# Kernel tuning notes

Measured on AMD Instinct MI355X. Metric: run time of the kernel, lower is better.

## Reference

```python
import jax, jax.numpy as jnp
import numpy as np

MARGIN = 0.3
NORM_EPS = 1e-12  # torch F.normalize default eps


def setup_inputs() -> dict:
    key = jax.random.key(0)
    k1, k2 = jax.random.split(key)
    embeddings = jax.random.normal(k1, (8192, 128), dtype=jnp.float32)
    labels = jax.random.randint(k2, (8192,), 0, 128, dtype=jnp.int64)
    return {"embeddings": embeddings, "labels": labels}


def _triplet_loss(embeddings, labels):
    # L2-normalize rows (torch F.normalize: x / max(||x||, eps))
    norm = jnp.linalg.norm(embeddings, axis=1, keepdims=True)
    e = embeddings / jnp.maximum(norm, NORM_EPS)

    # pairwise squared Euclidean via gram matrix
    dot = e @ e.T                     # [B, B]
    sq = jnp.diagonal(dot)            # [B]
    d2 = jnp.clip(sq[None, :] - 2.0 * dot + sq[:, None], 0.0)
    zmask = (d2 == 0.0).astype(d2.dtype)
    dist = jnp.sqrt(d2 + zmask * 1e-16) * (1.0 - zmask)  # [B, B]

    # hard mining, fully vectorized over rows
    same = labels[:, None] == labels[None, :]
    eye = jnp.eye(labels.shape[0], dtype=bool)
    pos_mask = same & ~eye
    neg_mask = ~same

    dist_ap = jnp.max(jnp.where(pos_mask, dist, -jnp.inf), axis=1)  # hardest positive
    dist_an = jnp.min(jnp.where(neg_mask, dist, jnp.inf), axis=1)   # hardest negative

    valid = pos_mask.any(axis=1) & neg_mask.any(axis=1)
    # MarginRankingLoss(margin)(dist_an, dist_ap, y=1) = mean relu(dist_ap - dist_an + margin)
    per_row = jnp.maximum(dist_ap - dist_an + MARGIN, 0.0)
    n_valid = jnp.maximum(jnp.sum(valid), 1).astype(dist.dtype)
    loss = jnp.sum(jnp.where(valid, per_row, 0.0)) / n_valid
    return jnp.where(valid.any(), loss, jnp.zeros((), dist.dtype))


def reference(embeddings, labels):
    return _triplet_loss(embeddings, labels)
```

## Files before the change

### kernel.cpp

```cpp
#include <hip/hip_runtime.h>
#include <cmath>

#define BN 8192
#define DIM 128
#define MARGIN_F 0.3f
#define NRB 64
#define NTILE (NRB * (NRB + 1) / 2)
#define NPART 64
#define IMAX 0x7FFFFFFF
#define IMIN 0x80000000

typedef __attribute__((ext_vector_type(4))) int i32x4;

__device__ __forceinline__ int imin3(int a, int b, int c) { return min(a, min(b, c)); }
__device__ __forceinline__ int imax3(int a, int b, int c) { return max(a, max(b, c)); }

__global__ __launch_bounds__(256) void norm_cvt_k(
    const float* __restrict__ emb, const int* __restrict__ lab,
    float* __restrict__ sqv, unsigned short* __restrict__ EnQ16,
    unsigned* __restrict__ LP)
{
  int gt = blockIdx.x * blockDim.x + threadIdx.x;
  if (gt < 2048) {
    int base = (gt >> 4) * 64 + (gt & 15);
    LP[gt] = (unsigned)(lab[base] & 255) | ((unsigned)(lab[base + 16] & 255) << 8) |
             ((unsigned)(lab[base + 32] & 255) << 16) | ((unsigned)(lab[base + 48] & 255) << 24);
  }

  int w = gt >> 6;
  int lane = threadIdx.x & 63;
  if (w >= BN) return;
  float2 v = *reinterpret_cast<const float2*>(&emb[w * DIM + lane * 2]);
  float s = v.x * v.x + v.y * v.y;
  #pragma unroll
  for (int off = 32; off > 0; off >>= 1) s += __shfl_xor(s, off);
  float iv = 1.0f / fmaxf(sqrtf(s), 1e-12f);
  if (lane == 0) sqv[w] = s * iv * iv;
  int q0 = (int)rintf(127.0f * v.x * iv);
  int q1 = (int)rintf(127.0f * v.y * iv);
  unsigned short us = (unsigned short)((q0 & 255) | ((q1 & 255) << 8));
  int g = lane >> 3;
  EnQ16[(g * BN + w) * 8 + (lane & 7)] = us;
}

__global__ __launch_bounds__(256, 2) void tri_gram_mine_k(
    const char* __restrict__ EnQ, const int* __restrict__ lab,
    const unsigned* __restrict__ LP,
    int* __restrict__ ap_part, int* __restrict__ an_part)
{
  __shared__ int sRP[2][128], sRN[2][128];
  __shared__ int sCP[2][128], sCN[2][128];

  const int tid = threadIdx.x;
  const int w = tid >> 6, l = tid & 63;
  const int wr = w >> 1, wc = w & 1;
  const int lrow = l & 15, lkg = l >> 4;

  const int idx = blockIdx.x;
  int R = (int)((129.0f - sqrtf(16641.0f - 8.0f * (float)idx)) * 0.5f);
  while (((R + 1) * (129 - (R + 1))) / 2 <= idx) ++R;
  while ((R * (129 - R)) / 2 > idx) --R;
  const int C = R + (idx - (R * (129 - R)) / 2);

  const int rowBase = R * 128 + wr * 64;
  const int colBase = C * 128 + wc * 64;
  const bool diagW  = (rowBase == colBase);
  const bool doCol  = (R != C);

  i32x4 a[4][2];
  #pragma unroll
  for (int mi = 0; mi < 4; ++mi)
    #pragma unroll
    for (int kk = 0; kk < 2; ++kk)
      a[mi][kk] = *reinterpret_cast<const i32x4*>(
          EnQ + (((size_t)((kk << 2) + lkg) * BN + rowBase + mi * 16 + lrow) << 4));

  int rlv[4][4];
  #pragma unroll
  for (int mi = 0; mi < 4; ++mi) {
    int rb = rowBase + mi * 16 + lkg * 4;
    #pragma unroll
    for (int r = 0; r < 4; ++r) rlv[mi][r] = lab[rb + r] & 255;
  }

  const unsigned LPv = LP[(colBase >> 6) * 16 + lrow];
  const int l0 = (int)(LPv & 255u),         l1 = (int)((LPv >> 8) & 255u);
  const int l2 = (int)((LPv >> 16) & 255u), l3 = (int)(LPv >> 24);

  int ap[4][4], an[4][4];
  #pragma unroll
  for (int mi = 0; mi < 4; ++mi)
    #pragma unroll
    for (int r = 0; r < 4; ++r) { ap[mi][r] = IMAX; an[mi][r] = IMIN; }
  int cmin[4], cmax[4];
  #pragma unroll
  for (int n = 0; n < 4; ++n) { cmin[n] = IMAX; cmax[n] = IMIN; }

  const i32x4 zf = {0, 0, 0, 0};

  const char* bp0 = EnQ + (((size_t)lkg * BN + colBase + lrow) << 4);
  const char* bp1 = bp0 + ((size_t)BN << 6);

  i32x4 b0[2][2], b1[2][2];
  #pragma unroll
  for (int n = 0; n < 2; ++n) {
    b0[0][n] = *reinterpret_cast<const i32x4*>(bp0 + n * 256);
    b0[1][n] = *reinterpret_cast<const i32x4*>(bp1 + n * 256);
    b1[0][n] = *reinterpret_cast<const i32x4*>(bp0 + (2 + n) * 256);
    b1[1][n] = *reinterpret_cast<const i32x4*>(bp1 + (2 + n) * 256);
  }

  i32x4 accA[4][2], accB[4][2];
  #pragma unroll
  for (int mi = 0; mi < 4; ++mi)
    #pragma unroll
    for (int n = 0; n < 2; ++n)
      accA[mi][n] = __builtin_amdgcn_mfma_i32_16x16x64_i8(a[mi][0], b0[0][n], zf, 0, 0, 0);
  #pragma unroll
  for (int mi = 0; mi < 4; ++mi)
    #pragma unroll
    for (int n = 0; n < 2; ++n)
      accA[mi][n] = __builtin_amdgcn_mfma_i32_16x16x64_i8(a[mi][1], b0[1][n], accA[mi][n], 0, 0, 0);
  #pragma unroll
  for (int mi = 0; mi < 4; ++mi)
    #pragma unroll
    for (int n = 0; n < 2; ++n)
      accB[mi][n] = __builtin_amdgcn_mfma_i32_16x16x64_i8(a[mi][0], b1[0][n], zf, 0, 0, 0);
  #pragma unroll
  for (int mi = 0; mi < 4; ++mi)
    #pragma unroll
    for (int n = 0; n < 2; ++n)
      accB[mi][n] = __builtin_amdgcn_mfma_i32_16x16x64_i8(a[mi][1], b1[1][n], accB[mi][n], 0, 0, 0);

  auto mineRow = [&](const i32x4 (&A)[4][2], int la, int lb) {
    #pragma unroll
    for (int mi = 0; mi < 4; ++mi)
      #pragma unroll
      for (int r = 0; r < 4; ++r) {
        int d0 = A[mi][0][r], d1 = A[mi][1][r];
        bool s0 = (rlv[mi][r] == la), s1 = (rlv[mi][r] == lb);
        int p0 = s0 ? d0 : IMAX, p1 = s1 ? d1 : IMAX;
        int q0 = s0 ? IMIN : d0, q1 = s1 ? IMIN : d1;
        ap[mi][r] = imin3(ap[mi][r], p0, p1);
        an[mi][r] = imax3(an[mi][r], q0, q1);
      }
  };
  auto mineRowCol = [&](const i32x4 (&A)[4][2], int la, int lb,
                        int& cmA, int& cxA, int& cmB, int& cxB) {
    #pragma unroll
    for (int mi = 0; mi < 4; ++mi)
      #pragma unroll
      for (int r = 0; r < 4; ++r) {
        int d0 = A[mi][0][r], d1 = A[mi][1][r];
        bool s0 = (rlv[mi][r] == la), s1 = (rlv[mi][r] == lb);
        int p0 = s0 ? d0 : IMAX, p1 = s1 ? d1 : IMAX;
        int q0 = s0 ? IMIN : d0, q1 = s1 ? IMIN : d1;
        ap[mi][r] = imin3(ap[mi][r], p0, p1);
        an[mi][r] = imax3(an[mi][r], q0, q1);
        cmA = min(cmA, p0); cxA = max(cxA, q0);
        cmB = min(cmB, p1); cxB = max(cxB, q1);
      }
  };
  auto mineDiag = [&](const i32x4 (&A)[4][2], int la, int lb, int c0, int c1) {
    #pragma unroll
    for (int mi = 0; mi < 4; ++mi)
      #pragma unroll
      for (int r = 0; r < 4; ++r) {
        int rloc = mi * 16 + lkg * 4 + r;
        int d0 = A[mi][0][r], d1 = A[mi][1][r];
        bool s0 = (rlv[mi][r] == la), s1 = (rlv[mi][r] == lb);
        bool e0 = (rloc == c0), e1 = (rloc == c1);
        int p0 = (s0 && !e0) ? d0 : IMAX, p1 = (s1 && !e1) ? d1 : IMAX;
        int q0 = s0 ? IMIN : d0, q1 = s1 ? IMIN : d1;
        ap[mi][r] = imin3(ap[mi][r], p0, p1);
        an[mi][r] = imax3(an[mi][r], q0, q1);
      }
  };

  if (diagW) {
    mineDiag(accA, l0, l1, lrow, 16 + lrow);
    mineDiag(accB, l2, l3, 32 + lrow, 48 + lrow);
  } else if (doCol) {
    mineRowCol(accA, l0, l1, cmin[0], cmax[0], cmin[1], cmax[1]);
    mineRowCol(accB, l2, l3, cmin[2], cmax[2], cmin[3], cmax[3]);
  } else {
    mineRow(accA, l0, l1);
    mineRow(accB, l2, l3);
  }

  #pragma unroll
  for (int mi = 0; mi < 4; ++mi)
    #pragma unroll
    for (int r = 0; r < 4; ++r) {
      int p = ap[mi][r], n = an[mi][r];
      #pragma unroll
      for (int off = 1; off < 16; off <<= 1) {
        p = min(p, __shfl_xor(p, off));
        n = max(n, __shfl_xor(n, off));
      }
      if (lrow == 0) {
        int rl = wr * 64 + mi * 16 + lkg * 4 + r;
        sRP[wc][rl] = p; sRN[wc][rl] = n;
      }
    }

  if (doCol) {
    #pragma unroll
    for (int n = 0; n < 4; ++n) {
      int cm = cmin[n], cx = cmax[n];
      cm = min(cm, __shfl_xor(cm, 16)); cm = min(cm, __shfl_xor(cm, 32));
      cx = max(cx, __shfl_xor(cx, 16)); cx = max(cx, __shfl_xor(cx, 32));
      if (lkg == 0) {
        int cl = wc * 64 + n * 16 + lrow;
        sCP[wr][cl] = cm; sCN[wr][cl] = cx;
      }
    }
  }

  __syncthreads();

  const int t = tid & 127;
  if (tid < 128) {
    int p = min(sRP[0][t], sRP[1][t]);
    int n = max(sRN[0][t], sRN[1][t]);
    ap_part[(size_t)C * BN + R * 128 + t] = p;
    an_part[(size_t)C * BN + R * 128 + t] = n;
  } else if (doCol) {
    int p = min(sCP[0][t], sCP[1][t]);
    int n = max(sCN[0][t], sCN[1][t]);
    ap_part[(size_t)R * BN + C * 128 + t] = p;
    an_part[(size_t)R * BN + C * 128 + t] = n;
  }
}

__global__ __launch_bounds__(256) void finalize_a_k(
    const int* __restrict__ ap_part, const int* __restrict__ an_part,
    const float* __restrict__ sqv,
    float* __restrict__ blk_sum, float* __restrict__ blk_cnt)
{
  __shared__ int sP[128], sN[128];
  __shared__ float ssum[4], scnt[4];
  const int tid = threadIdx.x;
  const int t = tid & 127, h = tid >> 7;
  const int r = blockIdx.x * 128 + t;

  int apt = IMAX, ant = IMIN;
  const int s0 = h * 32;
  #pragma unroll 8
  for (int s = 0; s < 32; ++s) {
    apt = min(apt, ap_part[(size_t)(s0 + s) * BN + r]);
    ant = max(ant, an_part[(size_t)(s0 + s) * BN + r]);
  }
  if (h) { sP[t] = apt; sN[t] = ant; }
  __syncthreads();

  float sum = 0.f, cnt = 0.f;
  if (!h) {
    apt = min(apt, sP[t]); ant = max(ant, sN[t]);
    if (apt != IMAX && ant != IMIN) {
      const float sc = 2.0f / (127.0f * 127.0f);
      float rs1 = sqv[r] + 1.0f;
      float dap = sqrtf(fmaxf(fmaf(-sc, (float)apt, rs1), 0.f));
      float dan = sqrtf(fmaxf(fmaf(-sc, (float)ant, rs1), 0.f));
      sum = fmaxf(dap - dan + MARGIN_F, 0.f);
      cnt = 1.f;
    }
  }
  #pragma unroll
  for (int off = 32; off > 0; off >>= 1) {
    sum += __shfl_xor(sum, off);
    cnt += __shfl_xor(cnt, off);
  }
  int wv = tid >> 6;
  if ((tid & 63) == 0) { ssum[wv] = sum; scnt[wv] = cnt; }
  __syncthreads();
  if (tid == 0) {
    blk_sum[blockIdx.x] = ssum[0] + ssum[1] + ssum[2] + ssum[3];
    blk_cnt[blockIdx.x] = scnt[0] + scnt[1] + scnt[2] + scnt[3];
  }
}

__global__ __launch_bounds__(64) void finalize_b_k(
    const float* __restrict__ blk_sum, const float* __restrict__ blk_cnt,
    float* __restrict__ out)
{
  int l = threadIdx.x;
  float s = blk_sum[l], c = blk_cnt[l];
  #pragma unroll
  for (int off = 32; off > 0; off >>= 1) {
    s += __shfl_xor(s, off);
    c += __shfl_xor(c, off);
  }
  if (l == 0) out[0] = (c > 0.f) ? (s / c) : 0.f;
}

extern "C" void kernel_launch(void* const* d_in, const int* in_sizes, int n_in,
                              void* d_out, int out_size, void* d_ws, size_t ws_size,
                              hipStream_t stream)
{
  const float* emb = (const float*)d_in[0];
  const int*   lab = (const int*)d_in[1];
  float* out = (float*)d_out;
  float* ws  = (float*)d_ws;

  float*    sqv     = ws;
  int*      ap_part = (int*)(sqv + BN);
  int*      an_part = ap_part + NPART * BN;
  float*    blk_sum = (float*)(an_part + NPART * BN);
  float*    blk_cnt = blk_sum + 64;
  unsigned* LP      = (unsigned*)(blk_cnt + 64);
  char*     EnQ     = (char*)(LP + 2048);

  norm_cvt_k<<<dim3(BN / 4), 256, 0, stream>>>(emb, lab, sqv, (unsigned short*)EnQ, LP);
  tri_gram_mine_k<<<dim3(NTILE), 256, 0, stream>>>(EnQ, lab, LP, ap_part, an_part);
  finalize_a_k<<<dim3(NRB), 256, 0, stream>>>(ap_part, an_part, sqv, blk_sum, blk_cnt);
  finalize_b_k<<<dim3(1), 64, 0, stream>>>(blk_sum, blk_cnt, out);
}
```

Baseline: 38.90 us.

## Replace per-tile triangular grid with paired row-strip blocks reusing A fragments

The gram/mining kernel now launches 32x16 blocks. Each block walks a contiguous chunk of upper-triangular tiles drawn from a pair of row blocks (p and 63-p) so the work is balanced. A-fragments and labels stay in registers across tiles in the same row block, and row partials are kept in registers and flushed once per row block into 32 slots rather than per tile. Column partials go to a separate buffer, and finalize now reads fewer row slots plus a variable number of column slots per row block. The trade-off is fewer, longer blocks with two block-wide syncs per off-diagonal tile, and less parallelism at launch.

Result: slower. 47.00 us (+20.8%).

```diff
diff --git a/kernel.cpp b/kernel.cpp
--- a/kernel.cpp
+++ b/kernel.cpp
@@ -5,8 +5,9 @@
 #define DIM 128
 #define MARGIN_F 0.3f
 #define NRB 64
-#define NTILE (NRB * (NRB + 1) / 2)
-#define NPART 64
+#define NPAIR 32
+#define NCHUNK 16
+#define NRSLOT (NCHUNK * 2)
 #define IMAX 0x7FFFFFFF
 #define IMIN 0x80000000
 
@@ -43,12 +44,12 @@
   EnQ16[(g * BN + w) * 8 + (lane & 7)] = us;
 }
 
-__global__ __launch_bounds__(256, 2) void tri_gram_mine_k(
+__global__ __launch_bounds__(256, 2) void tri_strip_mine_k(
     const char* __restrict__ EnQ, const int* __restrict__ lab,
     const unsigned* __restrict__ LP,
-    int* __restrict__ ap_part, int* __restrict__ an_part)
-{
-  __shared__ int sRP[2][128], sRN[2][128];
+    int* __restrict__ rp, int* __restrict__ rn,
+    int* __restrict__ cp, int* __restrict__ cn)
+{
   __shared__ int sCP[2][128], sCN[2][128];
 
   const int tid = threadIdx.x;
@@ -56,81 +57,57 @@
   const int wr = w >> 1, wc = w & 1;
   const int lrow = l & 15, lkg = l >> 4;
 
-  const int idx = blockIdx.x;
-  int R = (int)((129.0f - sqrtf(16641.0f - 8.0f * (float)idx)) * 0.5f);
-  while (((R + 1) * (129 - (R + 1))) / 2 <= idx) ++R;
-  while ((R * (129 - R)) / 2 > idx) --R;
-  const int C = R + (idx - (R * (129 - R)) / 2);
-
-  const int rowBase = R * 128 + wr * 64;
-  const int colBase = C * 128 + wc * 64;
-  const bool diagW  = (rowBase == colBase);
-  const bool doCol  = (R != C);
+  const int p = blockIdx.x, y = blockIdx.y;
+  const int rbB = 63 - p, lenA = 64 - p;
+  const int start = (y * 65) >> 4;
+  const int end   = ((y + 1) * 65) >> 4;
+  const int rslot = y * 2 + wc;
 
   i32x4 a[4][2];
-  #pragma unroll
-  for (int mi = 0; mi < 4; ++mi)
-    #pragma unroll
-    for (int kk = 0; kk < 2; ++kk)
-      a[mi][kk] = *reinterpret_cast<const i32x4*>(
-          EnQ + (((size_t)((kk << 2) + lkg) * BN + rowBase + mi * 16 + lrow) << 4));
-
   int rlv[4][4];
-  #pragma unroll
-  for (int mi = 0; mi < 4; ++mi) {
-    int rb = rowBase + mi * 16 + lkg * 4;
-    #pragma unroll
-    for (int r = 0; r < 4; ++r) rlv[mi][r] = lab[rb + r] & 255;
-  }
-
-  const unsigned LPv = LP[(colBase >> 6) * 16 + lrow];
-  const int l0 = (int)(LPv & 255u),         l1 = (int)((LPv >> 8) & 255u);
-  const int l2 = (int)((LPv >> 16) & 255u), l3 = (int)(LPv >> 24);
-
   int ap[4][4], an[4][4];
-  #pragma unroll
-  for (int mi = 0; mi < 4; ++mi)
-    #pragma unroll
-    for (int r = 0; r < 4; ++r) { ap[mi][r] = IMAX; an[mi][r] = IMIN; }
-  int cmin[4], cmax[4];
-  #pragma unroll
-  for (int n = 0; n < 4; ++n) { cmin[n] = IMAX; cmax[n] = IMIN; }
-
   const i32x4 zf = {0, 0, 0, 0};
 
-  const char* bp0 = EnQ + (((size_t)lkg * BN + colBase + lrow) << 4);
-  const char* bp1 = bp0 + ((size_t)BN << 6);
-
-  i32x4 b0[2][2], b1[2][2];
-  #pragma unroll
-  for (int n = 0; n < 2; ++n) {
-    b0[0][n] = *reinterpret_cast<const i32x4*>(bp0 + n * 256);
-    b0[1][n] = *reinterpret_cast<const i32x4*>(bp1 + n * 256);
-    b1[0][n] = *reinterpret_cast<const i32x4*>(bp0 + (2 + n) * 256);
-    b1[1][n] = *reinterpret_cast<const i32x4*>(bp1 + (2 + n) * 256);
-  }
-
-  i32x4 accA[4][2], accB[4][2];
-  #pragma unroll
-  for (int mi = 0; mi < 4; ++mi)
-    #pragma unroll
-    for (int n = 0; n < 2; ++n)
-      accA[mi][n] = __builtin_amdgcn_mfma_i32_16x16x64_i8(a[mi][0], b0[0][n], zf, 0, 0, 0);
-  #pragma unroll
-  for (int mi = 0; mi < 4; ++mi)
-    #pragma unroll
-    for (int n = 0; n < 2; ++n)
-      accA[mi][n] = __builtin_amdgcn_mfma_i32_16x16x64_i8(a[mi][1], b0[1][n], accA[mi][n], 0, 0, 0);
-  #pragma unroll
-  for (int mi = 0; mi < 4; ++mi)
-    #pragma unroll
-    for (int n = 0; n < 2; ++n)
-      accB[mi][n] = __builtin_amdgcn_mfma_i32_16x16x64_i8(a[mi][0], b1[0][n], zf, 0, 0, 0);
-  #pragma unroll
-  for (int mi = 0; mi < 4; ++mi)
-    #pragma unroll
-    for (int n = 0; n < 2; ++n)
-      accB[mi][n] = __builtin_amdgcn_mfma_i32_16x16x64_i8(a[mi][1], b1[1][n], accB[mi][n], 0, 0, 0);
+  auto resetAcc = [&]() {
+    #pragma unroll
+    for (int mi = 0; mi < 4; ++mi)
+      #pragma unroll
+      for (int r = 0; r < 4; ++r) { ap[mi][r] = IMAX; an[mi][r] = IMIN; }
+  };
+  auto loadRB = [&](int rb) {
+    const int rowBase = rb * 128 + wr * 64;
+    #pragma unroll
+    for (int mi = 0; mi < 4; ++mi)
+      #pragma unroll
+      for (int kk = 0; kk < 2; ++kk)
+        a[mi][kk] = *reinterpret_cast<const i32x4*>(
+            EnQ + (((size_t)((kk << 2) + lkg) * BN + rowBase + mi * 16 + lrow) << 4));
+    #pragma unroll
+    for (int mi = 0; mi < 4; ++mi) {
+      int rb8 = rowBase + mi * 16 + lkg * 4;
+      #pragma unroll
+      for (int r = 0; r < 4; ++r) rlv[mi][r] = lab[rb8 + r] & 255;
+    }
+    resetAcc();
+  };
+  auto flushRB = [&](int rb) {
+    #pragma unroll
+    for (int mi = 0; mi < 4; ++mi)
+      #pragma unroll
+      for (int r = 0; r < 4; ++r) {
+        int pp = ap[mi][r], nn = an[mi][r];
+        #pragma unroll
+        for (int off = 1; off < 16; off <<= 1) {
+          pp = min(pp, __shfl_xor(pp, off));
+          nn = max(nn, __shfl_xor(nn, off));
+        }
+        if (lrow == 0) {
+          int rg = rb * 128 + wr * 64 + mi * 16 + lkg * 4 + r;
+          rp[(size_t)rslot * BN + rg] = pp;
+          rn[(size_t)rslot * BN + rg] = nn;
+        }
+      }
+  };
 
   auto mineRow = [&](const i32x4 (&A)[4][2], int la, int lb) {
     #pragma unroll
@@ -177,79 +154,130 @@
       }
   };
 
-  if (diagW) {
-    mineDiag(accA, l0, l1, lrow, 16 + lrow);
-    mineDiag(accB, l2, l3, 32 + lrow, 48 + lrow);
-  } else if (doCol) {
-    mineRowCol(accA, l0, l1, cmin[0], cmax[0], cmin[1], cmax[1]);
-    mineRowCol(accB, l2, l3, cmin[2], cmax[2], cmin[3], cmax[3]);
-  } else {
-    mineRow(accA, l0, l1);
-    mineRow(accB, l2, l3);
-  }
-
-  #pragma unroll
-  for (int mi = 0; mi < 4; ++mi)
-    #pragma unroll
-    for (int r = 0; r < 4; ++r) {
-      int p = ap[mi][r], n = an[mi][r];
-      #pragma unroll
-      for (int off = 1; off < 16; off <<= 1) {
-        p = min(p, __shfl_xor(p, off));
-        n = max(n, __shfl_xor(n, off));
-      }
-      if (lrow == 0) {
-        int rl = wr * 64 + mi * 16 + lkg * 4 + r;
-        sRP[wc][rl] = p; sRN[wc][rl] = n;
-      }
-    }
-
-  if (doCol) {
-    #pragma unroll
-    for (int n = 0; n < 4; ++n) {
-      int cm = cmin[n], cx = cmax[n];
-      cm = min(cm, __shfl_xor(cm, 16)); cm = min(cm, __shfl_xor(cm, 32));
-      cx = max(cx, __shfl_xor(cx, 16)); cx = max(cx, __shfl_xor(cx, 32));
-      if (lkg == 0) {
-        int cl = wc * 64 + n * 16 + lrow;
-        sCP[wr][cl] = cm; sCN[wr][cl] = cx;
-      }
-    }
-  }
-
-  __syncthreads();
-
-  const int t = tid & 127;
-  if (tid < 128) {
-    int p = min(sRP[0][t], sRP[1][t]);
-    int n = max(sRN[0][t], sRN[1][t]);
-    ap_part[(size_t)C * BN + R * 128 + t] = p;
-    an_part[(size_t)C * BN + R * 128 + t] = n;
-  } else if (doCol) {
-    int p = min(sCP[0][t], sCP[1][t]);
-    int n = max(sCN[0][t], sCN[1][t]);
-    ap_part[(size_t)R * BN + C * 128 + t] = p;
-    an_part[(size_t)R * BN + C * 128 + t] = n;
-  }
+  int curRB = -1;
+  bool doneA = false, doneB = false;
+
+  #pragma unroll 1
+  for (int i = start; i < end; ++i) {
+    int R, C;
+    if (i < lenA) { R = p;   C = p + i; }
+    else          { R = rbB; C = rbB + (i - lenA); }
+
+    if (R != curRB) {
+      if (curRB == p) { flushRB(p); doneA = true; }
+      loadRB(R);
+      curRB = R;
+    }
+
+    const int colBase = C * 128 + wc * 64;
+    const bool diagBlk = (R == C);
+    const bool diagW = diagBlk && (wr == wc);
+
+    const unsigned LPv = LP[(C * 2 + wc) * 16 + lrow];
+    const int l0 = (int)(LPv & 255u),         l1 = (int)((LPv >> 8) & 255u);
+    const int l2 = (int)((LPv >> 16) & 255u), l3 = (int)(LPv >> 24);
+
+    const char* bp0 = EnQ + (((size_t)lkg * BN + colBase + lrow) << 4);
+    const char* bp1 = bp0 + ((size_t)BN << 6);
+    i32x4 b0[2][2], b1[2][2];
+    #pragma unroll
+    for (int n = 0; n < 2; ++n) {
+      b0[0][n] = *reinterpret_cast<const i32x4*>(bp0 + n * 256);
+      b0[1][n] = *reinterpret_cast<const i32x4*>(bp1 + n * 256);
+      b1[0][n] = *reinterpret_cast<const i32x4*>(bp0 + (2 + n) * 256);
+      b1[1][n] = *reinterpret_cast<const i32x4*>(bp1 + (2 + n) * 256);
+    }
+
+    i32x4 accA[4][2], accB[4][2];
+    #pragma unroll
+    for (int mi = 0; mi < 4; ++mi)
+      #pragma unroll
+      for (int n = 0; n < 2; ++n)
+        accA[mi][n] = __builtin_amdgcn_mfma_i32_16x16x64_i8(a[mi][0], b0[0][n], zf, 0, 0, 0);
+    #pragma unroll
+    for (int mi = 0; mi < 4; ++mi)
+      #pragma unroll
+      for (int n = 0; n < 2; ++n)
+        accA[mi][n] = __builtin_amdgcn_mfma_i32_16x16x64_i8(a[mi][1], b0[1][n], accA[mi][n], 0, 0, 0);
+    #pragma unroll
+    for (int mi = 0; mi < 4; ++mi)
+      #pragma unroll
+      for (int n = 0; n < 2; ++n)
+        accB[mi][n] = __builtin_amdgcn_mfma_i32_16x16x64_i8(a[mi][0], b1[0][n], zf, 0, 0, 0);
+    #pragma unroll
+    for (int mi = 0; mi < 4; ++mi)
+      #pragma unroll
+      for (int n = 0; n < 2; ++n)
+        accB[mi][n] = __builtin_amdgcn_mfma_i32_16x16x64_i8(a[mi][1], b1[1][n], accB[mi][n], 0, 0, 0);
+
+    int cmin[4], cmax[4];
+    #pragma unroll
+    for (int n = 0; n < 4; ++n) { cmin[n] = IMAX; cmax[n] = IMIN; }
+
+    if (diagW) {
+      mineDiag(accA, l0, l1, lrow, 16 + lrow);
+      mineDiag(accB, l2, l3, 32 + lrow, 48 + lrow);
+    } else if (!diagBlk) {
+      mineRowCol(accA, l0, l1, cmin[0], cmax[0], cmin[1], cmax[1]);
+      mineRowCol(accB, l2, l3, cmin[2], cmax[2], cmin[3], cmax[3]);
+    } else {
+      mineRow(accA, l0, l1);
+      mineRow(accB, l2, l3);
+    }
+
+    if (!diagBlk) {
+      #pragma unroll
+      for (int n = 0; n < 4; ++n) {
+        int cm = cmin[n], cx = cmax[n];
+        cm = min(cm, __shfl_xor(cm, 16)); cm = min(cm, __shfl_xor(cm, 32));
+        cx = max(cx, __shfl_xor(cx, 16)); cx = max(cx, __shfl_xor(cx, 32));
+        if (lkg == 0) {
+          int cl = wc * 64 + n * 16 + lrow;
+          sCP[wr][cl] = cm; sCN[wr][cl] = cx;
+        }
+      }
+      __syncthreads();
+      if (tid < 128) {
+        int pp = min(sCP[0][tid], sCP[1][tid]);
+        int nn = max(sCN[0][tid], sCN[1][tid]);
+        cp[(size_t)R * BN + C * 128 + tid] = pp;
+        cn[(size_t)R * BN + C * 128 + tid] = nn;
+      }
+      __syncthreads();
+    }
+  }
+
+  if (curRB == p)        { flushRB(p);   doneA = true; }
+  else if (curRB == rbB) { flushRB(rbB); doneB = true; }
+  if (!doneA) { resetAcc(); flushRB(p);   }
+  if (!doneB) { resetAcc(); flushRB(rbB); }
 }
 
 __global__ __launch_bounds__(256) void finalize_a_k(
-    const int* __restrict__ ap_part, const int* __restrict__ an_part,
+    const int* __restrict__ rp, const int* __restrict__ rn,
+    const int* __restrict__ cp, const int* __restrict__ cn,
     const float* __restrict__ sqv,
     float* __restrict__ blk_sum, float* __restrict__ blk_cnt)
 {
   __shared__ int sP[128], sN[128];
   __shared__ float ssum[4], scnt[4];
+  const int X = blockIdx.x;
   const int tid = threadIdx.x;
   const int t = tid & 127, h = tid >> 7;
-  const int r = blockIdx.x * 128 + t;
+  const int r = X * 128 + t;
 
   int apt = IMAX, ant = IMIN;
-  const int s0 = h * 32;
-  #pragma unroll 8
-  for (int s = 0; s < 32; ++s) {
-    apt = min(apt, ap_part[(size_t)(s0 + s) * BN + r]);
-    ant = max(ant, an_part[(size_t)(s0 + s) * BN + r]);
+  if (h == 0) {
+    #pragma unroll 8
+    for (int s = 0; s < NRSLOT; ++s) {
+      apt = min(apt, rp[(size_t)s * BN + r]);
+      ant = max(ant, rn[(size_t)s * BN + r]);
+    }
+  } else {
+    for (int s = 0; s < X; ++s) {
+      apt = min(apt, cp[(size_t)s * BN + r]);
+      ant = max(ant, cn[(size_t)s * BN + r]);
+    }
   }
   if (h) { sP[t] = apt; sN[t] = ant; }
   __syncthreads();
@@ -304,15 +332,17 @@
   float* ws  = (float*)d_ws;
 
   float*    sqv     = ws;
-  int*      ap_part = (int*)(sqv + BN);
-  int*      an_part = ap_part + NPART * BN;
-  float*    blk_sum = (float*)(an_part + NPART * BN);
+  int*      rp      = (int*)(sqv + BN);
+  int*      rn      = rp + (size_t)NRSLOT * BN;
+  int*      cp      = rn + (size_t)NRSLOT * BN;
+  int*      cn      = cp + (size_t)NRB * BN;
+  float*    blk_sum = (float*)(cn + (size_t)NRB * BN);
   float*    blk_cnt = blk_sum + 64;
   unsigned* LP      = (unsigned*)(blk_cnt + 64);
   char*     EnQ     = (char*)(LP + 2048);
 
   norm_cvt_k<<<dim3(BN / 4), 256, 0, stream>>>(emb, lab, sqv, (unsigned short*)EnQ, LP);
-  tri_gram_mine_k<<<dim3(NTILE), 256, 0, stream>>>(EnQ, lab, LP, ap_part, an_part);
-  finalize_a_k<<<dim3(NRB), 256, 0, stream>>>(ap_part, an_part, sqv, blk_sum, blk_cnt);
+  tri_strip_mine_k<<<dim3(NPAIR, NCHUNK), 256, 0, stream>>>(EnQ, lab, LP, rp, rn, cp, cn);
+  finalize_a_k<<<dim3(NRB), 256, 0, stream>>>(rp, rn, cp, cn, sqv, blk_sum, blk_cnt);
   finalize_b_k<<<dim3(1), 64, 0, stream>>>(blk_sum, blk_cnt, out);
 }
```
